# Optimization experiments

Hardware: AMD Instinct MI355X
Metric: run time of the kernel (lower is better)

## Reference

```python
import jax, jax.numpy as jnp
import numpy as np

N_NODES = 200_000
N_UND = 3_200_000        # undirected masked edges
E = 2 * N_UND            # directed edges


def _seg_mean(m, dst, n_nodes):
    # DGL fn.mean: mean over incoming edge messages; zero-in-degree nodes get 0.
    s = jax.ops.segment_sum(m, dst, num_segments=n_nodes)
    deg = jax.ops.segment_sum(jnp.ones((m.shape[0], 1), m.dtype), dst, num_segments=n_nodes)
    return s / jnp.maximum(deg, 1.0)


def setup_inputs() -> dict:
    key = jax.random.key(0)
    ks = jax.random.split(key, 18)
    w = lambda k, s: jax.random.normal(k, s, dtype=jnp.float32) * 0.1
    return {
        'node_feat': jax.random.normal(ks[0], (N_NODES, 7), dtype=jnp.float32),
        'edge_feat': jax.random.normal(ks[1], (E, 4), dtype=jnp.float32),
        'edge_mask': jax.random.normal(ks[2], (N_UND, 1), dtype=jnp.float32),
        'src': jax.random.randint(ks[3], (E,), 0, N_NODES),
        'dst': jax.random.randint(ks[4], (E,), 0, N_NODES),
        'W1a': w(ks[5], (11, 32)), 'b1a': jnp.zeros((32,), jnp.float32),
        'W1b': w(ks[6], (32, 32)), 'b1b': jnp.zeros((32,), jnp.float32),
        'W2a': w(ks[7], (32, 32)), 'b2a': jnp.zeros((32,), jnp.float32),
        'W2b': w(ks[8], (32, 32)), 'b2b': jnp.zeros((32,), jnp.float32),
        'Wm1': w(ks[9], (32, 16)), 'bm1': jnp.zeros((16,), jnp.float32),
        'Wm2': w(ks[10], (16, 2)), 'bm2': jnp.zeros((2,), jnp.float32),
    }


def reference(node_feat, edge_feat, edge_mask, src, dst,
              W1a, b1a, W1b, b1b, W2a, b2a, W2b, b2b, Wm1, bm1, Wm2, bm2):
    n_nodes = node_feat.shape[0]
    relu = jax.nn.relu
    # interleave mask to both edge directions: [m0, m0, m1, m1, ...]
    m_full = jax.nn.sigmoid(jnp.repeat(edge_mask, 2, axis=0))  # [E, 1]
    # layer 1: masked cat(edge_h, src_h) -> mean over dst -> MLP
    msg1 = m_full * jnp.concatenate([edge_feat, node_feat[src]], axis=1)  # [E, 11]
    h = _seg_mean(msg1, dst, n_nodes)                                      # [N, 11]
    h = relu(relu(h @ W1a + b1a) @ W1b + b1b)                              # [N, 32]
    # layer 2: masked src_h -> mean over dst -> MLP
    msg2 = m_full * h[src]                                                 # [E, 32]
    h = _seg_mean(msg2, dst, n_nodes)                                      # [N, 32]
    h = relu(relu(h @ W2a + b2a) @ W2b + b2b)                              # [N, 32]
    # global max pool + readout MLP + softmax (batch_size=1 path)
    g = jnp.max(h, axis=0)                                                 # [32]
    logits = relu(g @ Wm1 + bm1) @ Wm2 + bm2                               # [2]
    return jax.nn.softmax(logits)[None, :]                                 # [1, 2]
```

## Files before the change

kernel.cpp:

```cpp
#include <hip/hip_runtime.h>
#include <hip/hip_fp16.h>
#include <math.h>

#define SCHUNK 1024
#define PMAX   80
#define BSHIFT 9
#define MAXBKT 1024
#define BINB   1024
#define EPT    8

__device__ __forceinline__ float sigmoidf_(float x) {
    return 1.0f / (1.0f + __expf(-x));
}

union I2H { int i; __half2 h; };
__device__ __forceinline__ int pack_h2(float a, float b) {
    I2H u; u.h = __floats2half2_rn(a, b); return u.i;
}
__device__ __forceinline__ float2 unpack_h2(int w) {
    I2H u; u.i = w; return __half22float2(u.h);
}

typedef int v4i_nt __attribute__((ext_vector_type(4)));
typedef float v4f_nt __attribute__((ext_vector_type(4)));
__device__ __forceinline__ int4 ldnt16(const int4* p) {
    v4i_nt v = __builtin_nontemporal_load((const v4i_nt*)p);
    return make_int4(v[0], v[1], v[2], v[3]);
}
__device__ __forceinline__ float4 ldnt16f(const float* p) {
    v4f_nt v = __builtin_nontemporal_load((const v4f_nt*)p);
    return make_float4(v[0], v[1], v[2], v[3]);
}

__global__ void hist_rank(const int* __restrict__ dst, int* __restrict__ deg,
                          int* __restrict__ rank, int E) {
    int e = blockIdx.x * blockDim.x + threadIdx.x;
    if (e < E) rank[e] = atomicAdd(&deg[dst[e]], 1);
}

__global__ void scan_part(const int* __restrict__ deg, int* __restrict__ bsum, int N) {
    __shared__ int tot[256];
    int t = threadIdx.x;
    int base = blockIdx.x * SCHUNK + t * 4;
    int s = 0;
    if (base + 3 < N) {
        int4 v = *(const int4*)(deg + base);
        s = v.x + v.y + v.z + v.w;
    } else {
#pragma unroll
        for (int j = 0; j < 4; ++j) if (base + j < N) s += deg[base + j];
    }
    tot[t] = s;
    __syncthreads();
    for (int o = 128; o >= 1; o >>= 1) {
        if (t < o) tot[t] += tot[t + o];
        __syncthreads();
    }
    if (t == 0) bsum[blockIdx.x] = tot[0];
}

__global__ void scan_mid(int* __restrict__ bsum, int* __restrict__ off, int B, int N) {
    __shared__ int tmp[256];
    int t = threadIdx.x;
    int chunk = (B + 255) / 256;
    int lo = t * chunk, hi = min(lo + chunk, B);
    int s = 0;
    for (int i = lo; i < hi; ++i) s += bsum[i];
    tmp[t] = s;
    __syncthreads();
    for (int o = 1; o < 256; o <<= 1) {
        int v = (t >= o) ? tmp[t - o] : 0;
        __syncthreads();
        tmp[t] += v;
        __syncthreads();
    }
    int run = (t == 0) ? 0 : tmp[t - 1];
    for (int i = lo; i < hi; ++i) { int d = bsum[i]; bsum[i] = run; run += d; }
    if (t == 255) off[N] = tmp[255];
}

__global__ void scan_fin(const int* __restrict__ deg, const int* __restrict__ bsum,
                         int* __restrict__ off, int N) {
    __shared__ int tots[256];
    int t = threadIdx.x;
    int base = blockIdx.x * SCHUNK + t * 4;
    int v0 = 0, v1 = 0, v2 = 0, v3 = 0;
    if (base + 3 < N) {
        int4 v = *(const int4*)(deg + base);
        v0 = v.x; v1 = v.y; v2 = v.z; v3 = v.w;
    } else {
        if (base + 0 < N) v0 = deg[base + 0];
        if (base + 1 < N) v1 = deg[base + 1];
        if (base + 2 < N) v2 = deg[base + 2];
        if (base + 3 < N) v3 = deg[base + 3];
    }
    tots[t] = v0 + v1 + v2 + v3;
    __syncthreads();
    for (int o = 1; o < 256; o <<= 1) {
        int v = (t >= o) ? tots[t - o] : 0;
        __syncthreads();
        tots[t] += v;
        __syncthreads();
    }
    int run = bsum[blockIdx.x] + ((t == 0) ? 0 : tots[t - 1]);
    if (base + 0 < N) off[base + 0] = run; run += v0;
    if (base + 1 < N) off[base + 1] = run; run += v1;
    if (base + 2 < N) off[base + 2] = run; run += v2;
    if (base + 3 < N) off[base + 3] = run;
}

__global__ void pack_nodes(const float* __restrict__ nf, int4* __restrict__ nf16, int N) {
    int n = blockIdx.x * blockDim.x + threadIdx.x;
    if (n >= N) return;
    const float* p = nf + (size_t)n * 7;
    int4 w;
    w.x = pack_h2(p[0], p[1]);
    w.y = pack_h2(p[2], p[3]);
    w.z = pack_h2(p[4], p[5]);
    w.w = pack_h2(p[6], 0.0f);
    nf16[n] = w;
}

__global__ __launch_bounds__(BINB)
void binA(const int* __restrict__ dst, const int* __restrict__ src,
          const float* __restrict__ edge_mask, const float* __restrict__ edge_feat,
          const float* __restrict__ node_feat,
          int* __restrict__ bktCnt, int4* __restrict__ region, int4* __restrict__ nf16,
          int E, int N, int nbkt, int bcap) {
    __shared__ int cnt[MAXBKT];
    __shared__ int base[MAXBKT];
    int t = threadIdx.x;
    int gt = blockIdx.x * BINB + t;
    if (gt < N) {
        const float* p = node_feat + (size_t)gt * 7;
        int4 w;
        w.x = pack_h2(p[0], p[1]);
        w.y = pack_h2(p[2], p[3]);
        w.z = pack_h2(p[4], p[5]);
        w.w = pack_h2(p[6], 0.0f);
        nf16[gt] = w;
    }
    for (int i = t; i < nbkt; i += BINB) cnt[i] = 0;
    __syncthreads();
    int4 rec[EPT];
    int  bl[EPT];
    int e0 = blockIdx.x * (BINB * EPT) + t;
#pragma unroll
    for (int j = 0; j < EPT; ++j) {
        int e = e0 + j * BINB;
        bl[j] = -1;
        if (e < E) {
            int d = dst[e];
            int s = src[e];
            float m = sigmoidf_(edge_mask[e >> 1]);
            float4 ef = ldnt16f(edge_feat + (size_t)e * 4);
            int b = d >> BSHIFT;
            int dlo = d & ((1 << BSHIFT) - 1);
            int lr = atomicAdd(&cnt[b], 1);
            rec[j].x = (dlo << 18) | s;
            rec[j].y = pack_h2(m * ef.x, m * ef.y);
            rec[j].z = pack_h2(m * ef.z, m * ef.w);
            rec[j].w = __float_as_int(m);
            bl[j] = (b << 16) | lr;
        }
    }
    __syncthreads();
    for (int i = t; i < nbkt; i += BINB)
        base[i] = atomicAdd(&bktCnt[i], cnt[i]);
    __syncthreads();
#pragma unroll
    for (int j = 0; j < EPT; ++j) {
        if (bl[j] >= 0) {
            int b = bl[j] >> 16, lr = bl[j] & 0xffff;
            int pos = base[b] + lr;
            if (pos < bcap) region[(size_t)b * bcap + pos] = rec[j];
        }
    }
}

__global__ __launch_bounds__(1024)
void fillS(const int4* __restrict__ region, const int* __restrict__ bktCnt,
           int4* __restrict__ recP, int* __restrict__ deg, int N, int bcap) {
    __shared__ int cnt[1 << BSHIFT];
    int b = blockIdx.x;
    int t = threadIdx.x;
    if (t < (1 << BSHIFT)) cnt[t] = 0;
    __syncthreads();
    int count = min(bktCnt[b], bcap);
    const int4* reg = region + (size_t)b * bcap;
    int n0 = b << BSHIFT;
    for (int i = t; i < count; i += blockDim.x) {
        int4 w = ldnt16(reg + i);
        int dlo = ((unsigned)w.x) >> 18;
        int r = atomicAdd(&cnt[dlo], 1);
        if (r < PMAX) {
            w.x &= 0x3FFFF;
            recP[(size_t)(n0 + dlo) * PMAX + r] = w;
        }
    }
    __syncthreads();
    if (t < (1 << BSHIFT) && n0 + t < N) deg[n0 + t] = cnt[t];
}

__global__ void hist_fill_p(const int* __restrict__ dst, const int* __restrict__ src,
                            const float* __restrict__ edge_mask,
                            const float* __restrict__ edge_feat,
                            const float* __restrict__ node_feat,
                            int* __restrict__ deg, int4* __restrict__ recP,
                            int4* __restrict__ nf16, int E, int N) {
    int t = blockIdx.x * blockDim.x + threadIdx.x;
    if (t < N) {
        const float* p = node_feat + (size_t)t * 7;
        int4 w;
        w.x = pack_h2(p[0], p[1]);
        w.y = pack_h2(p[2], p[3]);
        w.z = pack_h2(p[4], p[5]);
        w.w = pack_h2(p[6], 0.0f);
        nf16[t] = w;
    }
    int e0 = blockIdx.x * (blockDim.x << 2) + threadIdx.x;
    int e1 = e0 + blockDim.x;
    int e2 = e1 + blockDim.x;
    int e3 = e2 + blockDim.x;
    bool v0 = e0 < E, v1 = e1 < E, v2 = e2 < E, v3 = e3 < E;
    int d0 = 0, d1 = 0, d2 = 0, d3 = 0;
    int s0 = 0, s1 = 0, s2 = 0, s3 = 0;
    float k0 = 0, k1 = 0, k2 = 0, k3 = 0;
    float4 f0 = {}, f1 = {}, f2 = {}, f3 = {};
    if (v0) { d0 = dst[e0]; s0 = src[e0]; k0 = edge_mask[e0 >> 1]; f0 = ldnt16f(edge_feat + (size_t)e0 * 4); }
    if (v1) { d1 = dst[e1]; s1 = src[e1]; k1 = edge_mask[e1 >> 1]; f1 = ldnt16f(edge_feat + (size_t)e1 * 4); }
    if (v2) { d2 = dst[e2]; s2 = src[e2]; k2 = edge_mask[e2 >> 1]; f2 = ldnt16f(edge_feat + (size_t)e2 * 4); }
    if (v3) { d3 = dst[e3]; s3 = src[e3]; k3 = edge_mask[e3 >> 1]; f3 = ldnt16f(edge_feat + (size_t)e3 * 4); }
    float m0 = sigmoidf_(k0), m1 = sigmoidf_(k1), m2 = sigmoidf_(k2), m3 = sigmoidf_(k3);
    int4 w0, w1, w2, w3;
    w0.x = s0; w0.y = pack_h2(m0 * f0.x, m0 * f0.y); w0.z = pack_h2(m0 * f0.z, m0 * f0.w); w0.w = __float_as_int(m0);
    w1.x = s1; w1.y = pack_h2(m1 * f1.x, m1 * f1.y); w1.z = pack_h2(m1 * f1.z, m1 * f1.w); w1.w = __float_as_int(m1);
    w2.x = s2; w2.y = pack_h2(m2 * f2.x, m2 * f2.y); w2.z = pack_h2(m2 * f2.z, m2 * f2.w); w2.w = __float_as_int(m2);
    w3.x = s3; w3.y = pack_h2(m3 * f3.x, m3 * f3.y); w3.z = pack_h2(m3 * f3.z, m3 * f3.w); w3.w = __float_as_int(m3);
    int r0 = 0, r1 = 0, r2 = 0, r3 = 0;
    if (v0) r0 = atomicAdd(&deg[d0], 1);
    if (v1) r1 = atomicAdd(&deg[d1], 1);
    if (v2) r2 = atomicAdd(&deg[d2], 1);
    if (v3) r3 = atomicAdd(&deg[d3], 1);
    if (v0 && r0 < PMAX) recP[(size_t)d0 * PMAX + r0] = w0;
    if (v1 && r1 < PMAX) recP[(size_t)d1 * PMAX + r1] = w1;
    if (v2 && r2 < PMAX) recP[(size_t)d2 * PMAX + r2] = w2;
    if (v3 && r3 < PMAX) recP[(size_t)d3 * PMAX + r3] = w3;
}

__global__ void agg1_p(const int4* __restrict__ recP, const int* __restrict__ degv,
                       const int4* __restrict__ nf16,
                       const float* __restrict__ W1a, const float* __restrict__ b1a,
                       const float* __restrict__ W1b, const float* __restrict__ b1b,
                       __half* __restrict__ h1h, int N) {
    __shared__ float sW1a[11 * 32], sb1a[32], sW1b[32 * 32], sb1b[32];
    for (int i = threadIdx.x; i < 11 * 32; i += blockDim.x) sW1a[i] = W1a[i];
    for (int i = threadIdx.x; i < 32 * 32; i += blockDim.x) sW1b[i] = W1b[i];
    if (threadIdx.x < 32) { sb1a[threadIdx.x] = b1a[threadIdx.x]; sb1b[threadIdx.x] = b1b[threadIdx.x]; }
    __syncthreads();
    int n = blockIdx.x * (blockDim.x >> 2) + (threadIdx.x >> 2);
    int sub = threadIdx.x & 3;
    int deg = 0;
    size_t start = 0;
    if (n < N) { deg = degv[n]; start = (size_t)n * PMAX; }
    int dd = min(deg, PMAX);
    float x[11];
#pragma unroll
    for (int j = 0; j < 11; ++j) x[j] = 0.0f;
    int i = sub;
    for (; i + 4 < dd; i += 8) {
        int4 r0 = ldnt16(recP + start + i);
        int4 r1 = ldnt16(recP + start + i + 4);
        int4 nw0 = nf16[r0.x];
        int4 nw1 = nf16[r1.x];
        {
            float m = __int_as_float(r0.w);
            float2 e01 = unpack_h2(r0.y), e23 = unpack_h2(r0.z);
            x[0] += e01.x; x[1] += e01.y; x[2] += e23.x; x[3] += e23.y;
            float2 n01 = unpack_h2(nw0.x), n23 = unpack_h2(nw0.y);
            float2 n45 = unpack_h2(nw0.z), n6 = unpack_h2(nw0.w);
            x[4] += m * n01.x; x[5]  += m * n01.y; x[6] += m * n23.x; x[7] += m * n23.y;
            x[8] += m * n45.x; x[9]  += m * n45.y; x[10] += m * n6.x;
        }
        {
// ... 82 lines not shown
        const int4* hp1 = (const int4*)(h1h + (size_t)r1.x * 32);
        int4 g00 = hp0[0], g01 = hp0[1], g02 = hp0[2], g03 = hp0[3];
        int4 g10 = hp1[0], g11 = hp1[1], g12 = hp1[2], g13 = hp1[3];
        {
            float m = __int_as_float(r0.w);
            float2 a, b, c, d;
            a = unpack_h2(g00.x); b = unpack_h2(g00.y); c = unpack_h2(g00.z); d = unpack_h2(g00.w);
            x[0] += m * a.x; x[1] += m * a.y; x[2] += m * b.x; x[3] += m * b.y;
            x[4] += m * c.x; x[5] += m * c.y; x[6] += m * d.x; x[7] += m * d.y;
            a = unpack_h2(g01.x); b = unpack_h2(g01.y); c = unpack_h2(g01.z); d = unpack_h2(g01.w);
            x[8] += m * a.x; x[9] += m * a.y; x[10] += m * b.x; x[11] += m * b.y;
            x[12] += m * c.x; x[13] += m * c.y; x[14] += m * d.x; x[15] += m * d.y;
            a = unpack_h2(g02.x); b = unpack_h2(g02.y); c = unpack_h2(g02.z); d = unpack_h2(g02.w);
            x[16] += m * a.x; x[17] += m * a.y; x[18] += m * b.x; x[19] += m * b.y;
            x[20] += m * c.x; x[21] += m * c.y; x[22] += m * d.x; x[23] += m * d.y;
            a = unpack_h2(g03.x); b = unpack_h2(g03.y); c = unpack_h2(g03.z); d = unpack_h2(g03.w);
            x[24] += m * a.x; x[25] += m * a.y; x[26] += m * b.x; x[27] += m * b.y;
            x[28] += m * c.x; x[29] += m * c.y; x[30] += m * d.x; x[31] += m * d.y;
        }
        {
            float m = __int_as_float(r1.w);
            float2 a, b, c, d;
            a = unpack_h2(g10.x); b = unpack_h2(g10.y); c = unpack_h2(g10.z); d = unpack_h2(g10.w);
            x[0] += m * a.x; x[1] += m * a.y; x[2] += m * b.x; x[3] += m * b.y;
            x[4] += m * c.x; x[5] += m * c.y; x[6] += m * d.x; x[7] += m * d.y;
            a = unpack_h2(g11.x); b = unpack_h2(g11.y); c = unpack_h2(g11.z); d = unpack_h2(g11.w);
            x[8] += m * a.x; x[9] += m * a.y; x[10] += m * b.x; x[11] += m * b.y;
            x[12] += m * c.x; x[13] += m * c.y; x[14] += m * d.x; x[15] += m * d.y;
            a = unpack_h2(g12.x); b = unpack_h2(g12.y); c = unpack_h2(g12.z); d = unpack_h2(g12.w);
            x[16] += m * a.x; x[17] += m * a.y; x[18] += m * b.x; x[19] += m * b.y;
            x[20] += m * c.x; x[21] += m * c.y; x[22] += m * d.x; x[23] += m * d.y;
            a = unpack_h2(g13.x); b = unpack_h2(g13.y); c = unpack_h2(g13.z); d = unpack_h2(g13.w);
            x[24] += m * a.x; x[25] += m * a.y; x[26] += m * b.x; x[27] += m * b.y;
            x[28] += m * c.x; x[29] += m * c.y; x[30] += m * d.x; x[31] += m * d.y;
        }
    }
    for (; i < dd; i += 4) {
        int4 r = ldnt16(recP + start + i);
        float m = __int_as_float(r.w);
        const int4* hp = (const int4*)(h1h + (size_t)r.x * 32);
#pragma unroll
        for (int q = 0; q < 4; ++q) {
            int4 v = hp[q];
            float2 a = unpack_h2(v.x), b = unpack_h2(v.y);
            float2 c = unpack_h2(v.z), d = unpack_h2(v.w);
            x[8 * q + 0] += m * a.x; x[8 * q + 1] += m * a.y;
            x[8 * q + 2] += m * b.x; x[8 * q + 3] += m * b.y;
            x[8 * q + 4] += m * c.x; x[8 * q + 5] += m * c.y;
            x[8 * q + 6] += m * d.x; x[8 * q + 7] += m * d.y;
        }
    }
#pragma unroll
    for (int j = 0; j < 32; ++j) {
        x[j] += __shfl_xor(x[j], 1);
        x[j] += __shfl_xor(x[j], 2);
    }
    float inv = 1.0f / fmaxf((float)deg, 1.0f);
#pragma unroll
    for (int j = 0; j < 32; ++j) x[j] *= inv;
    float hdn[32];
#pragma unroll
    for (int k = 0; k < 32; ++k) {
        float acc = sb2a[k];
#pragma unroll
        for (int j = 0; j < 32; ++j) acc += x[j] * sW2a[j * 32 + k];
        hdn[k] = fmaxf(acc, 0.0f);
    }
    int lane = threadIdx.x & 63;
#pragma unroll
    for (int k2 = 0; k2 < 32; ++k2) {
        float acc = sb2b[k2];
#pragma unroll
        for (int k = 0; k < 32; ++k) acc += hdn[k] * sW2b[k * 32 + k2];
        float v = valid ? fmaxf(acc, 0.0f) : 0.0f;
#pragma unroll
        for (int o = 32; o >= 1; o >>= 1)
            v = fmaxf(v, __shfl_xor(v, o));
        if (lane == 0) atomicMax(&smax[k2], __float_as_int(v));
    }
    __syncthreads();
    if (threadIdx.x < 32) atomicMax((int*)&gmax[threadIdx.x], smax[threadIdx.x]);
}

__global__ void fill_rec16(const int* __restrict__ dst, const int* __restrict__ rank,
                           const int* __restrict__ off,
                           const float* __restrict__ edge_mask,
                           const int* __restrict__ src,
                           const float* __restrict__ edge_feat,
                           int4* __restrict__ rec, int E) {
    int e = blockIdx.x * blockDim.x + threadIdx.x;
    if (e >= E) return;
    int p = off[dst[e]] + rank[e];
    float m = sigmoidf_(edge_mask[e >> 1]);
    float4 ef = ldnt16f(edge_feat + (size_t)e * 4);
    int4 w;
    w.x = src[e];
    w.y = pack_h2(m * ef.x, m * ef.y);
    w.z = pack_h2(m * ef.z, m * ef.w);
    w.w = __float_as_int(m);
    rec[p] = w;
}

__global__ void agg1_16(const int4* __restrict__ rec, const int* __restrict__ off,
                        const int4* __restrict__ nf16,
                        const float* __restrict__ W1a, const float* __restrict__ b1a,
                        const float* __restrict__ W1b, const float* __restrict__ b1b,
                        __half* __restrict__ h1h, int N) {
    __shared__ float sW1a[11 * 32], sb1a[32], sW1b[32 * 32], sb1b[32];
    for (int i = threadIdx.x; i < 11 * 32; i += blockDim.x) sW1a[i] = W1a[i];
    for (int i = threadIdx.x; i < 32 * 32; i += blockDim.x) sW1b[i] = W1b[i];
    if (threadIdx.x < 32) { sb1a[threadIdx.x] = b1a[threadIdx.x]; sb1b[threadIdx.x] = b1b[threadIdx.x]; }
    __syncthreads();
    int n = blockIdx.x * (blockDim.x >> 2) + (threadIdx.x >> 2);
    int sub = threadIdx.x & 3;
    int start = 0, deg = 0;
    if (n < N) { start = off[n]; deg = off[n + 1] - start; }
    float x[11];
#pragma unroll
    for (int j = 0; j < 11; ++j) x[j] = 0.0f;
    for (int i = sub; i < deg; i += 4) {
        int4 r = ldnt16(rec + start + i);
        float m = __int_as_float(r.w);
        float2 e01 = unpack_h2(r.y), e23 = unpack_h2(r.z);
        x[0] += e01.x; x[1] += e01.y; x[2] += e23.x; x[3] += e23.y;
        int4 nw = nf16[r.x];
        float2 n01 = unpack_h2(nw.x), n23 = unpack_h2(nw.y);
        float2 n45 = unpack_h2(nw.z), n6 = unpack_h2(nw.w);
        x[4] += m * n01.x; x[5]  += m * n01.y; x[6] += m * n23.x; x[7] += m * n23.y;
        x[8] += m * n45.x; x[9]  += m * n45.y; x[10] += m * n6.x;
    }
#pragma unroll
    for (int j = 0; j < 11; ++j) {
        x[j] += __shfl_xor(x[j], 1);
        x[j] += __shfl_xor(x[j], 2);
    }
    if (n >= N) return;
    float inv = 1.0f / fmaxf((float)deg, 1.0f);
#pragma unroll
    for (int j = 0; j < 11; ++j) x[j] *= inv;
    float hdn[32];
#pragma unroll
    for (int k = 0; k < 32; ++k) {
        float acc = sb1a[k];
#pragma unroll
        for (int j = 0; j < 11; ++j) acc += x[j] * sW1a[j * 32 + k];
        hdn[k] = fmaxf(acc, 0.0f);
    }
    float o[32];
#pragma unroll
    for (int k2 = 0; k2 < 32; ++k2) {
        float acc = sb1b[k2];
#pragma unroll
        for (int k = 0; k < 32; ++k) acc += hdn[k] * sW1b[k * 32 + k2];
        o[k2] = fmaxf(acc, 0.0f);
    }
    int4 w;
    w.x = pack_h2(o[8 * sub + 0], o[8 * sub + 1]);
    w.y = pack_h2(o[8 * sub + 2], o[8 * sub + 3]);
    w.z = pack_h2(o[8 * sub + 4], o[8 * sub + 5]);
    w.w = pack_h2(o[8 * sub + 6], o[8 * sub + 7]);
    ((int4*)(h1h + (size_t)n * 32))[sub] = w;
}

__global__ void agg2_16(const int4* __restrict__ rec, const int* __restrict__ off,
                        const __half* __restrict__ h1h,
                        const float* __restrict__ W2a, const float* __restrict__ b2a,
                        const float* __restrict__ W2b, const float* __restrict__ b2b,
                        float* __restrict__ gmax, int N) {
    __shared__ float sW2a[32 * 32], sb2a[32], sW2b[32 * 32], sb2b[32];
    __shared__ int smax[32];
    for (int i = threadIdx.x; i < 32 * 32; i += blockDim.x) { sW2a[i] = W2a[i]; sW2b[i] = W2b[i]; }
    if (threadIdx.x < 32) {
        sb2a[threadIdx.x] = b2a[threadIdx.x];
        sb2b[threadIdx.x] = b2b[threadIdx.x];
        smax[threadIdx.x] = 0;
    }
    __syncthreads();
    int n = blockIdx.x * (blockDim.x >> 2) + (threadIdx.x >> 2);
    int sub = threadIdx.x & 3;
    bool valid = (n < N);
    int start = 0, deg = 0;
    if (valid) { start = off[n]; deg = off[n + 1] - start; }
    float x[32];
#pragma unroll
    for (int j = 0; j < 32; ++j) x[j] = 0.0f;
    for (int i = sub; i < deg; i += 4) {
        int4 r = ldnt16(rec + start + i);
        float m = __int_as_float(r.w);
        const int4* hp = (const int4*)(h1h + (size_t)r.x * 32);
#pragma unroll
        for (int q = 0; q < 4; ++q) {
            int4 v = hp[q];
            float2 a = unpack_h2(v.x), b = unpack_h2(v.y);
            float2 c = unpack_h2(v.z), d = unpack_h2(v.w);
            x[8 * q + 0] += m * a.x; x[8 * q + 1] += m * a.y;
            x[8 * q + 2] += m * b.x; x[8 * q + 3] += m * b.y;
            x[8 * q + 4] += m * c.x; x[8 * q + 5] += m * c.y;
            x[8 * q + 6] += m * d.x; x[8 * q + 7] += m * d.y;
        }
    }
#pragma unroll
    for (int j = 0; j < 32; ++j) {
        x[j] += __shfl_xor(x[j], 1);
        x[j] += __shfl_xor(x[j], 2);
    }
    float inv = 1.0f / fmaxf((float)deg, 1.0f);
#pragma unroll
    for (int j = 0; j < 32; ++j) x[j] *= inv;
    float hdn[32];
#pragma unroll
    for (int k = 0; k < 32; ++k) {
        float acc = sb2a[k];
#pragma unroll
        for (int j = 0; j < 32; ++j) acc += x[j] * sW2a[j * 32 + k];
        hdn[k] = fmaxf(acc, 0.0f);
    }
    int lane = threadIdx.x & 63;
#pragma unroll
    for (int k2 = 0; k2 < 32; ++k2) {
        float acc = sb2b[k2];
#pragma unroll
        for (int k = 0; k < 32; ++k) acc += hdn[k] * sW2b[k * 32 + k2];
        float v = valid ? fmaxf(acc, 0.0f) : 0.0f;
#pragma unroll
        for (int o = 32; o >= 1; o >>= 1)
            v = fmaxf(v, __shfl_xor(v, o));
        if (lane == 0) atomicMax(&smax[k2], __float_as_int(v));
    }
    __syncthreads();
    if (threadIdx.x < 32) atomicMax((int*)&gmax[threadIdx.x], smax[threadIdx.x]);
}

__global__ void fill_rec(const int* __restrict__ dst, const int* __restrict__ rank,
                         const int* __restrict__ off,
                         const float* __restrict__ edge_mask,
                         const int* __restrict__ src,
                         int2* __restrict__ rec, int E) {
    int e = blockIdx.x * blockDim.x + threadIdx.x;
    if (e >= E) return;
    int p = off[dst[e]] + rank[e];
    float m = sigmoidf_(edge_mask[e >> 1]);
    int mq = (int)(m * 16384.0f + 0.5f);
    mq = min(mq, 16383);
    unsigned packed = ((unsigned)src[e] << 14) | (unsigned)mq;
    rec[p] = make_int2(e, (int)packed);
}

__global__ void agg1_rec(const int2* __restrict__ rec, const int* __restrict__ off,
                         const float* __restrict__ edge_feat,
                         const float* __restrict__ node_feat,
                         const float* __restrict__ W1a, const float* __restrict__ b1a,
                         const float* __restrict__ W1b, const float* __restrict__ b1b,
                         float* __restrict__ h1, int N) {
    __shared__ float sW1a[11 * 32], sb1a[32], sW1b[32 * 32], sb1b[32];
    for (int i = threadIdx.x; i < 11 * 32; i += blockDim.x) sW1a[i] = W1a[i];
    for (int i = threadIdx.x; i < 32 * 32; i += blockDim.x) sW1b[i] = W1b[i];
    if (threadIdx.x < 32) { sb1a[threadIdx.x] = b1a[threadIdx.x]; sb1b[threadIdx.x] = b1b[threadIdx.x]; }
    __syncthreads();
    int n = blockIdx.x * blockDim.x + threadIdx.x;
    if (n >= N) return;
    int start = off[n];
    int deg = off[n + 1] - start;
    float x[11];
#pragma unroll
    for (int j = 0; j < 11; ++j) x[j] = 0.0f;
    for (int i = 0; i < deg; ++i) {
        int2 r = rec[start + i];
        int e = r.x;
        unsigned packed = (unsigned)r.y;
        int s = (int)(packed >> 14);
        float m = (float)(packed & 16383u) * (1.0f / 16384.0f);
        float4 ef = *(const float4*)(edge_feat + (size_t)e * 4);
        x[0] += m * ef.x; x[1] += m * ef.y; x[2] += m * ef.z; x[3] += m * ef.w;
        const float* nf = node_feat + (size_t)s * 7;
#pragma unroll
        for (int j = 0; j < 7; ++j) x[4 + j] += m * nf[j];
    }
    float inv = 1.0f / fmaxf((float)deg, 1.0f);
#pragma unroll
    for (int j = 0; j < 11; ++j) x[j] *= inv;
    float hdn[32];
#pragma unroll
    for (int k = 0; k < 32; ++k) {
        float acc = sb1a[k];
#pragma unroll
        for (int j = 0; j < 11; ++j) acc += x[j] * sW1a[j * 32 + k];
        hdn[k] = fmaxf(acc, 0.0f);
    }
    float o[32];
#pragma unroll
    for (int k2 = 0; k2 < 32; ++k2) {
        float acc = sb1b[k2];
#pragma unroll
        for (int k = 0; k < 32; ++k) acc += hdn[k] * sW1b[k * 32 + k2];
        o[k2] = fmaxf(acc, 0.0f);
    }
    float4* outp = (float4*)(h1 + (size_t)n * 32);
#pragma unroll
    for (int q = 0; q < 8; ++q)
        outp[q] = make_float4(o[4 * q], o[4 * q + 1], o[4 * q + 2], o[4 * q + 3]);
}

__global__ void agg2_rec(const int2* __restrict__ rec, const int* __restrict__ off,
                         const float* __restrict__ h1,
                         const float* __restrict__ W2a, const float* __restrict__ b2a,
                         const float* __restrict__ W2b, const float* __restrict__ b2b,
                         float* __restrict__ gmax, int N) {
    __shared__ float sW2a[32 * 32], sb2a[32], sW2b[32 * 32], sb2b[32];
    __shared__ int smax[32];
    for (int i = threadIdx.x; i < 32 * 32; i += blockDim.x) { sW2a[i] = W2a[i]; sW2b[i] = W2b[i]; }
    if (threadIdx.x < 32) {
        sb2a[threadIdx.x] = b2a[threadIdx.x];
        sb2b[threadIdx.x] = b2b[threadIdx.x];
        smax[threadIdx.x] = 0;
    }
// ... 17 lines not shown
            float4 v = hp[q];
            x[4 * q + 0] += m * v.x;
            x[4 * q + 1] += m * v.y;
            x[4 * q + 2] += m * v.z;
            x[4 * q + 3] += m * v.w;
        }
    }
    float inv = 1.0f / fmaxf((float)deg, 1.0f);
#pragma unroll
    for (int j = 0; j < 32; ++j) x[j] *= inv;
    float hdn[32];
#pragma unroll
    for (int k = 0; k < 32; ++k) {
        float acc = sb2a[k];
#pragma unroll
        for (int j = 0; j < 32; ++j) acc += x[j] * sW2a[j * 32 + k];
        hdn[k] = fmaxf(acc, 0.0f);
    }
    int lane = threadIdx.x & 63;
#pragma unroll
    for (int k2 = 0; k2 < 32; ++k2) {
        float acc = sb2b[k2];
#pragma unroll
        for (int k = 0; k < 32; ++k) acc += hdn[k] * sW2b[k * 32 + k2];
        float v = valid ? fmaxf(acc, 0.0f) : 0.0f;
#pragma unroll
        for (int o = 32; o >= 1; o >>= 1)
            v = fmaxf(v, __shfl_xor(v, o));
        if (lane == 0) atomicMax(&smax[k2], __float_as_int(v));
    }
    __syncthreads();
    if (threadIdx.x < 32) atomicMax((int*)&gmax[threadIdx.x], smax[threadIdx.x]);
}

__global__ void readout(const float* __restrict__ gmax,
                        const float* __restrict__ Wm1, const float* __restrict__ bm1,
                        const float* __restrict__ Wm2, const float* __restrict__ bm2,
                        float* __restrict__ out) {
    __shared__ float p[16];
    int t = threadIdx.x;
    if (t < 16) {
        float acc = bm1[t];
        for (int j = 0; j < 32; ++j) acc += gmax[j] * Wm1[j * 16 + t];
        p[t] = fmaxf(acc, 0.0f);
    }
    __syncthreads();
    if (t == 0) {
        float l0 = bm2[0], l1 = bm2[1];
        for (int k = 0; k < 16; ++k) { l0 += p[k] * Wm2[k * 2]; l1 += p[k] * Wm2[k * 2 + 1]; }
        float mx = fmaxf(l0, l1);
        float e0 = __expf(l0 - mx), e1 = __expf(l1 - mx);
        float s = e0 + e1;
        out[0] = e0 / s;
        out[1] = e1 / s;
    }
}

static inline size_t align16(size_t x) { return (x + 15) & ~(size_t)15; }

extern "C" void kernel_launch(void* const* d_in, const int* in_sizes, int n_in,
                              void* d_out, int out_size, void* d_ws, size_t ws_size,
                              hipStream_t stream) {
    const float* node_feat = (const float*)d_in[0];
    const float* edge_feat = (const float*)d_in[1];
    const float* edge_mask = (const float*)d_in[2];
    const int*   src       = (const int*)d_in[3];
    const int*   dst       = (const int*)d_in[4];
    const float* W1a = (const float*)d_in[5];
    const float* b1a = (const float*)d_in[6];
    const float* W1b = (const float*)d_in[7];
    const float* b1b = (const float*)d_in[8];
    const float* W2a = (const float*)d_in[9];
    const float* b2a = (const float*)d_in[10];
    const float* W2b = (const float*)d_in[11];
    const float* b2b = (const float*)d_in[12];
    const float* Wm1 = (const float*)d_in[13];
    const float* bm1 = (const float*)d_in[14];
    const float* Wm2 = (const float*)d_in[15];
    const float* bm2 = (const float*)d_in[16];

    const int N = in_sizes[0] / 7;
    const int E = in_sizes[3];
    const int B = (N + SCHUNK - 1) / SCHUNK;

    {
        const int nbkt = (N + (1 << BSHIFT) - 1) >> BSHIFT;
        if (nbkt <= MAXBKT && N <= (1 << 18)) {
            int avg = (E + nbkt - 1) / nbkt;
            int bcap = avg + avg / 8 + 256;
            char* basep = (char*)d_ws;
            size_t off0 = 0;
            int*   bktCnt = (int*)(basep + off0);  off0 += (size_t)(nbkt + 32) * sizeof(int);
            float* gmax   = (float*)(bktCnt + nbkt);
            off0 = align16(off0);
            int*   degS   = (int*)(basep + off0);  off0 += (size_t)N * sizeof(int);
            off0 = align16(off0);
            int4*  nf16   = (int4*)(basep + off0); off0 += (size_t)N * sizeof(int4);
            int4*  recP   = (int4*)(basep + off0); off0 += (size_t)N * PMAX * sizeof(int4);
            int4*  region = (int4*)(basep + off0);
            __half* h1h   = (__half*)region;
            size_t regionBytes = (size_t)nbkt * bcap * sizeof(int4);
            size_t h1Bytes = (size_t)N * 32 * sizeof(__half);
            off0 += (regionBytes > h1Bytes ? regionBytes : h1Bytes);
            const size_t needS = off0;
            if (ws_size >= needS) {
                hipMemsetAsync(d_ws, 0, (size_t)(nbkt + 32) * sizeof(int), stream);
                const int binBlocks = (max(E, N) + BINB * EPT - 1) / (BINB * EPT);
                binA<<<binBlocks, BINB, 0, stream>>>(dst, src, edge_mask, edge_feat, node_feat,
                                                     bktCnt, region, nf16, E, N, nbkt, bcap);
                fillS<<<nbkt, 1024, 0, stream>>>(region, bktCnt, recP, degS, N, bcap);
                const int nodeBlocks = (N + 63) / 64;
                agg1_p<<<nodeBlocks, 256, 0, stream>>>(recP, degS, nf16,
                                                       W1a, b1a, W1b, b1b, h1h, N);
                agg2_p<<<nodeBlocks, 256, 0, stream>>>(recP, degS, h1h,
                                                       W2a, b2a, W2b, b2b, gmax, N);
                readout<<<1, 64, 0, stream>>>(gmax, Wm1, bm1, Wm2, bm2, (float*)d_out);
                return;
            }
        }
    }

    {
        int*    deg_i = (int*)d_ws;
        float*  gmax  = (float*)(deg_i + N);
        __half* h1h   = (__half*)(gmax + 32);
        int4*   nf16  = (int4*)(h1h + (size_t)N * 32);
        int4*   recP  = nf16 + N;
        const size_t needP = (size_t)(deg_i + N + 32 - (int*)d_ws) * sizeof(int)
                           + (size_t)N * 32 * sizeof(__half)
                           + (size_t)N * sizeof(int4)
                           + (size_t)N * PMAX * sizeof(int4);
        if (ws_size >= needP) {
            hipMemsetAsync(d_ws, 0, (size_t)(N + 32) * sizeof(int), stream);
            int threadsNeeded = max((E + 3) / 4, N);
            const int gridEF = (threadsNeeded + 255) / 256;
            hist_fill_p<<<gridEF, 256, 0, stream>>>(dst, src, edge_mask, edge_feat,
                                                    node_feat, deg_i, recP, nf16, E, N);
            const int nodeBlocks = (N + 63) / 64;
            agg1_p<<<nodeBlocks, 256, 0, stream>>>(recP, deg_i, nf16,
                                                   W1a, b1a, W1b, b1b, h1h, N);
            agg2_p<<<nodeBlocks, 256, 0, stream>>>(recP, deg_i, h1h,
                                                   W2a, b2a, W2b, b2b, gmax, N);
            readout<<<1, 64, 0, stream>>>(gmax, Wm1, bm1, Wm2, bm2, (float*)d_out);
            return;
        }
    }

    int*   deg_i = (int*)d_ws;
    float* gmax  = (float*)(deg_i + N);
    int*   off   = (int*)(gmax + 32);
    int*   bsum  = off + (N + 1);
    int*   slot  = bsum + (B + 1);

    const size_t slot16 = (size_t)E > (size_t)16 * N ? (size_t)E : (size_t)16 * N;
    int*    rank   = slot;
    __half* h1h    = (__half*)slot;
    int4*   rec16  = (int4*)(slot + slot16);
    int4*   nf16   = rec16 + E;
    const size_t need16 = ((size_t)2 * N + 34 + B + slot16 + (size_t)E * 4 + (size_t)N * 4) * sizeof(int);

    const size_t slot8 = (size_t)E > (size_t)32 * N ? (size_t)E : (size_t)32 * N;
    float* h1f  = (float*)slot;
    int2*  rec8 = (int2*)(slot + slot8);

    hipMemsetAsync(d_ws, 0, (size_t)(N + 32) * sizeof(int), stream);

    hist_rank<<<(E + 255) / 256, 256, 0, stream>>>(dst, deg_i, rank, E);
    scan_part<<<B, 256, 0, stream>>>(deg_i, bsum, N);
    scan_mid<<<1, 256, 0, stream>>>(bsum, off, B, N);
    scan_fin<<<B, 256, 0, stream>>>(deg_i, bsum, off, N);

    if (ws_size >= need16) {
        const int nodeBlocks = (N + 63) / 64;
        pack_nodes<<<(N + 255) / 256, 256, 0, stream>>>(node_feat, nf16, N);
        fill_rec16<<<(E + 255) / 256, 256, 0, stream>>>(dst, rank, off, edge_mask, src,
                                                        edge_feat, rec16, E);
        agg1_16<<<nodeBlocks, 256, 0, stream>>>(rec16, off, nf16,
                                                W1a, b1a, W1b, b1b, h1h, N);
        agg2_16<<<nodeBlocks, 256, 0, stream>>>(rec16, off, h1h,
                                                W2a, b2a, W2b, b2b, gmax, N);
    } else {
        fill_rec<<<(E + 255) / 256, 256, 0, stream>>>(dst, rank, off, edge_mask, src, rec8, E);
        agg1_rec<<<(N + 255) / 256, 256, 0, stream>>>(rec8, off, edge_feat, node_feat,
                                                      W1a, b1a, W1b, b1b, h1f, N);
        agg2_rec<<<(N + 255) / 256, 256, 0, stream>>>(rec8, off, h1f,
                                                      W2a, b2a, W2b, b2b, gmax, N);
    }
    readout<<<1, 64, 0, stream>>>(gmax, Wm1, bm1, Wm2, bm2, (float*)d_out);
}
```

Before: 668.3 us.

## Aggregate directly from dst buckets with LDS atomics, dropping the per-node fill pass

Adds agg1R/agg2R, which have one 1024-thread block per 512-node destination bucket. Each block reads the binned edge records straight from the bucket region and accumulates messages and degree into shared-memory rows with float atomics, then runs the per-node MLPs. This removes the fillS scatter into a padded per-node record array (N*PMAX int4) and its extra global traffic, and also lifts the PMAX cap on in-degree. In exchange it adds heavy LDS atomic contention (up to 33 atomics per edge in layer 2), uses only 512 of 1024 threads for the MLP phase, and makes float summation order nondeterministic. It also deletes the unused rec16 fallback path.

```diff
diff --git a/kernel.cpp b/kernel.cpp
--- a/kernel.cpp
+++ b/kernel.cpp
@@ -5,6 +5,7 @@
 #define SCHUNK 1024
 #define PMAX   80
 #define BSHIFT 9
+#define RB     (1 << BSHIFT)
 #define MAXBKT 1024
 #define BINB   1024
 #define EPT    8
@@ -107,18 +108,6 @@
     if (base + 1 < N) off[base + 1] = run; run += v1;
     if (base + 2 < N) off[base + 2] = run; run += v2;
     if (base + 3 < N) off[base + 3] = run;
-}
-
-__global__ void pack_nodes(const float* __restrict__ nf, int4* __restrict__ nf16, int N) {
-    int n = blockIdx.x * blockDim.x + threadIdx.x;
-    if (n >= N) return;
-    const float* p = nf + (size_t)n * 7;
-    int4 w;
-    w.x = pack_h2(p[0], p[1]);
-    w.y = pack_h2(p[2], p[3]);
-    w.z = pack_h2(p[4], p[5]);
-    w.w = pack_h2(p[6], 0.0f);
-    nf16[n] = w;
 }
 
 __global__ __launch_bounds__(BINB)
@@ -155,7 +144,7 @@
             float m = sigmoidf_(edge_mask[e >> 1]);
             float4 ef = ldnt16f(edge_feat + (size_t)e * 4);
             int b = d >> BSHIFT;
-            int dlo = d & ((1 << BSHIFT) - 1);
+            int dlo = d & (RB - 1);
             int lr = atomicAdd(&cnt[b], 1);
             rec[j].x = (dlo << 18) | s;
             rec[j].y = pack_h2(m * ef.x, m * ef.y);
@@ -179,12 +168,168 @@
 }
 
 __global__ __launch_bounds__(1024)
+void agg1R(const int4* __restrict__ region, const int* __restrict__ bktCnt,
+           const int4* __restrict__ nf16,
+           const float* __restrict__ W1a, const float* __restrict__ b1a,
+           const float* __restrict__ W1b, const float* __restrict__ b1b,
+           __half* __restrict__ h1h, int N, int bcap) {
+    __shared__ float xs[RB * 13];
+    __shared__ float sW1a[11 * 32], sb1a[32], sW1b[32 * 32], sb1b[32];
+    int t = threadIdx.x;
+    for (int i = t; i < 11 * 32; i += 1024) sW1a[i] = W1a[i];
+    for (int i = t; i < 32 * 32; i += 1024) sW1b[i] = W1b[i];
+    if (t < 32) { sb1a[t] = b1a[t]; sb1b[t] = b1b[t]; }
+    for (int i = t; i < RB * 13; i += 1024) xs[i] = 0.0f;
+    __syncthreads();
+    int b = blockIdx.x;
+    int count = min(bktCnt[b], bcap);
+    const int4* reg = region + (size_t)b * bcap;
+    for (int i = t; i < count; i += 1024) {
+        int4 w = ldnt16(reg + i);
+        int dlo = ((unsigned)w.x) >> 18;
+        int s = w.x & 0x3FFFF;
+        float m = __int_as_float(w.w);
+        float2 e01 = unpack_h2(w.y), e23 = unpack_h2(w.z);
+        int4 nw = nf16[s];
+        float2 n01 = unpack_h2(nw.x), n23 = unpack_h2(nw.y);
+        float2 n45 = unpack_h2(nw.z), n6 = unpack_h2(nw.w);
+        float* xp = xs + dlo * 13;
+        atomicAdd(xp + 0, e01.x);  atomicAdd(xp + 1, e01.y);
+        atomicAdd(xp + 2, e23.x);  atomicAdd(xp + 3, e23.y);
+        atomicAdd(xp + 4, m * n01.x);  atomicAdd(xp + 5, m * n01.y);
+        atomicAdd(xp + 6, m * n23.x);  atomicAdd(xp + 7, m * n23.y);
+        atomicAdd(xp + 8, m * n45.x);  atomicAdd(xp + 9, m * n45.y);
+        atomicAdd(xp + 10, m * n6.x);
+        atomicAdd(xp + 11, 1.0f);
+    }
+    __syncthreads();
+    int n0 = b << BSHIFT;
+    if (t < RB && n0 + t < N) {
+        float inv = 1.0f / fmaxf(xs[t * 13 + 11], 1.0f);
+        float hdn[32];
+#pragma unroll
+        for (int k = 0; k < 32; ++k) hdn[k] = sb1a[k];
+#pragma unroll
+        for (int j = 0; j < 11; ++j) {
+            float xv = xs[t * 13 + j] * inv;
+#pragma unroll
+            for (int k = 0; k < 32; ++k) hdn[k] += xv * sW1a[j * 32 + k];
+        }
+#pragma unroll
+        for (int k = 0; k < 32; ++k) hdn[k] = fmaxf(hdn[k], 0.0f);
+        int4* outp = (int4*)(h1h + (size_t)(n0 + t) * 32);
+#pragma unroll
+        for (int q = 0; q < 4; ++q) {
+            float o0 = sb1b[q * 8 + 0], o1 = sb1b[q * 8 + 1], o2 = sb1b[q * 8 + 2], o3 = sb1b[q * 8 + 3];
+            float o4 = sb1b[q * 8 + 4], o5 = sb1b[q * 8 + 5], o6 = sb1b[q * 8 + 6], o7 = sb1b[q * 8 + 7];
+#pragma unroll
+            for (int k = 0; k < 32; ++k) {
+                float hk = hdn[k];
+                const float* wr = sW1b + k * 32 + q * 8;
+                o0 += hk * wr[0]; o1 += hk * wr[1]; o2 += hk * wr[2]; o3 += hk * wr[3];
+                o4 += hk * wr[4]; o5 += hk * wr[5]; o6 += hk * wr[6]; o7 += hk * wr[7];
+            }
+            int4 w;
+            w.x = pack_h2(fmaxf(o0, 0.0f), fmaxf(o1, 0.0f));
+            w.y = pack_h2(fmaxf(o2, 0.0f), fmaxf(o3, 0.0f));
+            w.z = pack_h2(fmaxf(o4, 0.0f), fmaxf(o5, 0.0f));
+            w.w = pack_h2(fmaxf(o6, 0.0f), fmaxf(o7, 0.0f));
+            outp[q] = w;
+        }
+    }
+}
+
+__global__ __launch_bounds__(1024)
+void agg2R(const int4* __restrict__ region, const int* __restrict__ bktCnt,
+           const __half* __restrict__ h1h,
+           const float* __restrict__ W2a, const float* __restrict__ b2a,
+           const float* __restrict__ W2b, const float* __restrict__ b2b,
+           float* __restrict__ gmax, int N, int bcap) {
+    __shared__ float xs[RB * 33];
+    __shared__ float sW2a[32 * 32], sb2a[32], sW2b[32 * 32], sb2b[32];
+    __shared__ int smax[32];
+    int t = threadIdx.x;
+    for (int i = t; i < 32 * 32; i += 1024) { sW2a[i] = W2a[i]; sW2b[i] = W2b[i]; }
+    if (t < 32) { sb2a[t] = b2a[t]; sb2b[t] = b2b[t]; smax[t] = 0; }
+    for (int i = t; i < RB * 33; i += 1024) xs[i] = 0.0f;
+    __syncthreads();
+    int b = blockIdx.x;
+    int count = min(bktCnt[b], bcap);
+    const int4* reg = region + (size_t)b * bcap;
+    for (int i = t; i < count; i += 1024) {
+        int4 w = ldnt16(reg + i);
+        int dlo = ((unsigned)w.x) >> 18;
+        int s = w.x & 0x3FFFF;
+        float m = __int_as_float(w.w);
+        const int4* hp = (const int4*)(h1h + (size_t)s * 32);
+        int4 g0 = hp[0], g1 = hp[1], g2 = hp[2], g3 = hp[3];
+        float* xp = xs + dlo * 33;
+        float2 a, c;
+        a = unpack_h2(g0.x); c = unpack_h2(g0.y);
+        atomicAdd(xp + 0, m * a.x); atomicAdd(xp + 1, m * a.y);
+        atomicAdd(xp + 2, m * c.x); atomicAdd(xp + 3, m * c.y);
+        a = unpack_h2(g0.z); c = unpack_h2(g0.w);
+        atomicAdd(xp + 4, m * a.x); atomicAdd(xp + 5, m * a.y);
+        atomicAdd(xp + 6, m * c.x); atomicAdd(xp + 7, m * c.y);
+        a = unpack_h2(g1.x); c = unpack_h2(g1.y);
+        atomicAdd(xp + 8, m * a.x); atomicAdd(xp + 9, m * a.y);
+        atomicAdd(xp + 10, m * c.x); atomicAdd(xp + 11, m * c.y);
+        a = unpack_h2(g1.z); c = unpack_h2(g1.w);
+        atomicAdd(xp + 12, m * a.x); atomicAdd(xp + 13, m * a.y);
+        atomicAdd(xp + 14, m * c.x); atomicAdd(xp + 15, m * c.y);
+        a = unpack_h2(g2.x); c = unpack_h2(g2.y);
+        atomicAdd(xp + 16, m * a.x); atomicAdd(xp + 17, m * a.y);
+        atomicAdd(xp + 18, m * c.x); atomicAdd(xp + 19, m * c.y);
+        a = unpack_h2(g2.z); c = unpack_h2(g2.w);
+        atomicAdd(xp + 20, m * a.x); atomicAdd(xp + 21, m * a.y);
+        atomicAdd(xp + 22, m * c.x); atomicAdd(xp + 23, m * c.y);
+        a = unpack_h2(g3.x); c = unpack_h2(g3.y);
+        atomicAdd(xp + 24, m * a.x); atomicAdd(xp + 25, m * a.y);
+        atomicAdd(xp + 26, m * c.x); atomicAdd(xp + 27, m * c.y);
+        a = unpack_h2(g3.z); c = unpack_h2(g3.w);
+        atomicAdd(xp + 28, m * a.x); atomicAdd(xp + 29, m * a.y);
+        atomicAdd(xp + 30, m * c.x); atomicAdd(xp + 31, m * c.y);
+        atomicAdd(xp + 32, 1.0f);
+    }
+    __syncthreads();
+    int n0 = b << BSHIFT;
+    if (t < RB) {
+        bool valid = (n0 + t < N);
+        float inv = 1.0f / fmaxf(xs[t * 33 + 32], 1.0f);
+        float hdn[32];
+#pragma unroll
+        for (int k = 0; k < 32; ++k) hdn[k] = sb2a[k];
+#pragma unroll
+        for (int j = 0; j < 32; ++j) {
+            float xv = xs[t * 33 + j] * inv;
+#pragma unroll
+            for (int k = 0; k < 32; ++k) hdn[k] += xv * sW2a[j * 32 + k];
+        }
+#pragma unroll
+        for (int k = 0; k < 32; ++k) hdn[k] = fmaxf(hdn[k], 0.0f);
+#pragma unroll
+        for (int k2 = 0; k2 < 32; ++k2) {
+            float acc = sb2b[k2];
+#pragma unroll
+            for (int k = 0; k < 32; ++k) acc += hdn[k] * sW2b[k * 32 + k2];
+            float v = valid ? fmaxf(acc, 0.0f) : 0.0f;
+#pragma unroll
+            for (int o = 32; o >= 1; o >>= 1)
+                v = fmaxf(v, __shfl_xor(v, o));
+            if ((t & 63) == 0) atomicMax(&smax[k2], __float_as_int(v));
+        }
+    }
+    __syncthreads();
+    if (t < 32) atomicMax((int*)&gmax[t], smax[t]);
+}
+
+__global__ __launch_bounds__(1024)
 void fillS(const int4* __restrict__ region, const int* __restrict__ bktCnt,
            int4* __restrict__ recP, int* __restrict__ deg, int N, int bcap) {
-    __shared__ int cnt[1 << BSHIFT];
+    __shared__ int cnt[RB];
     int b = blockIdx.x;
     int t = threadIdx.x;
-    if (t < (1 << BSHIFT)) cnt[t] = 0;
+    if (t < RB) cnt[t] = 0;
     __syncthreads();
     int count = min(bktCnt[b], bcap);
     const int4* reg = region + (size_t)b * bcap;
@@ -199,7 +344,7 @@
         }
     }
     __syncthreads();
-    if (t < (1 << BSHIFT) && n0 + t < N) deg[n0 + t] = cnt[t];
+    if (t < RB && n0 + t < N) deg[n0 + t] = cnt[t];
 }
 
 __global__ void hist_fill_p(const int* __restrict__ dst, const int* __restrict__ src,
@@ -448,155 +593,6 @@
     if (threadIdx.x < 32) atomicMax((int*)&gmax[threadIdx.x], smax[threadIdx.x]);
 }
 
-__global__ void fill_rec16(const int* __restrict__ dst, const int* __restrict__ rank,
-                           const int* __restrict__ off,
-                           const float* __restrict__ edge_mask,
-                           const int* __restrict__ src,
-                           const float* __restrict__ edge_feat,
-                           int4* __restrict__ rec, int E) {
-    int e = blockIdx.x * blockDim.x + threadIdx.x;
-    if (e >= E) return;
-    int p = off[dst[e]] + rank[e];
-    float m = sigmoidf_(edge_mask[e >> 1]);
-    float4 ef = ldnt16f(edge_feat + (size_t)e * 4);
-    int4 w;
-    w.x = src[e];
-    w.y = pack_h2(m * ef.x, m * ef.y);
-    w.z = pack_h2(m * ef.z, m * ef.w);
-    w.w = __float_as_int(m);
-    rec[p] = w;
-}
-
-__global__ void agg1_16(const int4* __restrict__ rec, const int* __restrict__ off,
-                        const int4* __restrict__ nf16,
-                        const float* __restrict__ W1a, const float* __restrict__ b1a,
-                        const float* __restrict__ W1b, const float* __restrict__ b1b,
-                        __half* __restrict__ h1h, int N) {
-    __shared__ float sW1a[11 * 32], sb1a[32], sW1b[32 * 32], sb1b[32];
-    for (int i = threadIdx.x; i < 11 * 32; i += blockDim.x) sW1a[i] = W1a[i];
-    for (int i = threadIdx.x; i < 32 * 32; i += blockDim.x) sW1b[i] = W1b[i];
-    if (threadIdx.x < 32) { sb1a[threadIdx.x] = b1a[threadIdx.x]; sb1b[threadIdx.x] = b1b[threadIdx.x]; }
-    __syncthreads();
-    int n = blockIdx.x * (blockDim.x >> 2) + (threadIdx.x >> 2);
-    int sub = threadIdx.x & 3;
-    int start = 0, deg = 0;
-    if (n < N) { start = off[n]; deg = off[n + 1] - start; }
-    float x[11];
-#pragma unroll
-    for (int j = 0; j < 11; ++j) x[j] = 0.0f;
-    for (int i = sub; i < deg; i += 4) {
-        int4 r = ldnt16(rec + start + i);
-        float m = __int_as_float(r.w);
-        float2 e01 = unpack_h2(r.y), e23 = unpack_h2(r.z);
-        x[0] += e01.x; x[1] += e01.y; x[2] += e23.x; x[3] += e23.y;
-        int4 nw = nf16[r.x];
-        float2 n01 = unpack_h2(nw.x), n23 = unpack_h2(nw.y);
-        float2 n45 = unpack_h2(nw.z), n6 = unpack_h2(nw.w);
-        x[4] += m * n01.x; x[5]  += m * n01.y; x[6] += m * n23.x; x[7] += m * n23.y;
-        x[8] += m * n45.x; x[9]  += m * n45.y; x[10] += m * n6.x;
-    }
-#pragma unroll
-    for (int j = 0; j < 11; ++j) {
-        x[j] += __shfl_xor(x[j], 1);
-        x[j] += __shfl_xor(x[j], 2);
-    }
-    if (n >= N) return;
-    float inv = 1.0f / fmaxf((float)deg, 1.0f);
-#pragma unroll
-    for (int j = 0; j < 11; ++j) x[j] *= inv;
-    float hdn[32];
-#pragma unroll
-    for (int k = 0; k < 32; ++k) {
-        float acc = sb1a[k];
-#pragma unroll
-        for (int j = 0; j < 11; ++j) acc += x[j] * sW1a[j * 32 + k];
-        hdn[k] = fmaxf(acc, 0.0f);
-    }
-    float o[32];
-#pragma unroll
-    for (int k2 = 0; k2 < 32; ++k2) {
-        float acc = sb1b[k2];
-#pragma unroll
-        for (int k = 0; k < 32; ++k) acc += hdn[k] * sW1b[k * 32 + k2];
-        o[k2] = fmaxf(acc, 0.0f);
-    }
-    int4 w;
-    w.x = pack_h2(o[8 * sub + 0], o[8 * sub + 1]);
-    w.y = pack_h2(o[8 * sub + 2], o[8 * sub + 3]);
-    w.z = pack_h2(o[8 * sub + 4], o[8 * sub + 5]);
-    w.w = pack_h2(o[8 * sub + 6], o[8 * sub + 7]);
-    ((int4*)(h1h + (size_t)n * 32))[sub] = w;
-}
-
-__global__ void agg2_16(const int4* __restrict__ rec, const int* __restrict__ off,
-                        const __half* __restrict__ h1h,
-                        const float* __restrict__ W2a, const float* __restrict__ b2a,
-                        const float* __restrict__ W2b, const float* __restrict__ b2b,
-                        float* __restrict__ gmax, int N) {
-    __shared__ float sW2a[32 * 32], sb2a[32], sW2b[32 * 32], sb2b[32];
-    __shared__ int smax[32];
-    for (int i = threadIdx.x; i < 32 * 32; i += blockDim.x) { sW2a[i] = W2a[i]; sW2b[i] = W2b[i]; }
-    if (threadIdx.x < 32) {
-        sb2a[threadIdx.x] = b2a[threadIdx.x];
-        sb2b[threadIdx.x] = b2b[threadIdx.x];
-        smax[threadIdx.x] = 0;
-    }
-    __syncthreads();
-    int n = blockIdx.x * (blockDim.x >> 2) + (threadIdx.x >> 2);
-    int sub = threadIdx.x & 3;
-    bool valid = (n < N);
-    int start = 0, deg = 0;
-    if (valid) { start = off[n]; deg = off[n + 1] - start; }
-    float x[32];
-#pragma unroll
-    for (int j = 0; j < 32; ++j) x[j] = 0.0f;
-    for (int i = sub; i < deg; i += 4) {
-        int4 r = ldnt16(rec + start + i);
-        float m = __int_as_float(r.w);
-        const int4* hp = (const int4*)(h1h + (size_t)r.x * 32);
-#pragma unroll
-        for (int q = 0; q < 4; ++q) {
-            int4 v = hp[q];
-            float2 a = unpack_h2(v.x), b = unpack_h2(v.y);
-            float2 c = unpack_h2(v.z), d = unpack_h2(v.w);
-            x[8 * q + 0] += m * a.x; x[8 * q + 1] += m * a.y;
-            x[8 * q + 2] += m * b.x; x[8 * q + 3] += m * b.y;
-            x[8 * q + 4] += m * c.x; x[8 * q + 5] += m * c.y;
-            x[8 * q + 6] += m * d.x; x[8 * q + 7] += m * d.y;
-        }
-    }
-#pragma unroll
-    for (int j = 0; j < 32; ++j) {
-        x[j] += __shfl_xor(x[j], 1);
-        x[j] += __shfl_xor(x[j], 2);
-    }
-    float inv = 1.0f / fmaxf((float)deg, 1.0f);
-#pragma unroll
-    for (int j = 0; j < 32; ++j) x[j] *= inv;
-    float hdn[32];
-#pragma unroll
-    for (int k = 0; k < 32; ++k) {
-        float acc = sb2a[k];
-#pragma unroll
-        for (int j = 0; j < 32; ++j) acc += x[j] * sW2a[j * 32 + k];
-        hdn[k] = fmaxf(acc, 0.0f);
-    }
-    int lane = threadIdx.x & 63;
-#pragma unroll
-    for (int k2 = 0; k2 < 32; ++k2) {
-        float acc = sb2b[k2];
-#pragma unroll
-        for (int k = 0; k < 32; ++k) acc += hdn[k] * sW2b[k * 32 + k2];
-        float v = valid ? fmaxf(acc, 0.0f) : 0.0f;
-#pragma unroll
-        for (int o = 32; o >= 1; o >>= 1)
-            v = fmaxf(v, __shfl_xor(v, o));
-        if (lane == 0) atomicMax(&smax[k2], __float_as_int(v));
-    }
-    __syncthreads();
-    if (threadIdx.x < 32) atomicMax((int*)&gmax[threadIdx.x], smax[threadIdx.x]);
-}
-
 __global__ void fill_rec(const int* __restrict__ dst, const int* __restrict__ rank,
                          const int* __restrict__ off,
                          const float* __restrict__ edge_mask,
@@ -780,41 +776,64 @@
     const int N = in_sizes[0] / 7;
     const int E = in_sizes[3];
     const int B = (N + SCHUNK - 1) / SCHUNK;
-
-    {
-        const int nbkt = (N + (1 << BSHIFT) - 1) >> BSHIFT;
-        if (nbkt <= MAXBKT && N <= (1 << 18)) {
-            int avg = (E + nbkt - 1) / nbkt;
-            int bcap = avg + avg / 8 + 256;
-            char* basep = (char*)d_ws;
-            size_t off0 = 0;
-            int*   bktCnt = (int*)(basep + off0);  off0 += (size_t)(nbkt + 32) * sizeof(int);
-            float* gmax   = (float*)(bktCnt + nbkt);
-            off0 = align16(off0);
-            int*   degS   = (int*)(basep + off0);  off0 += (size_t)N * sizeof(int);
-            off0 = align16(off0);
-            int4*  nf16   = (int4*)(basep + off0); off0 += (size_t)N * sizeof(int4);
-            int4*  recP   = (int4*)(basep + off0); off0 += (size_t)N * PMAX * sizeof(int4);
-            int4*  region = (int4*)(basep + off0);
-            __half* h1h   = (__half*)region;
-            size_t regionBytes = (size_t)nbkt * bcap * sizeof(int4);
-            size_t h1Bytes = (size_t)N * 32 * sizeof(__half);
-            off0 += (regionBytes > h1Bytes ? regionBytes : h1Bytes);
-            const size_t needS = off0;
-            if (ws_size >= needS) {
-                hipMemsetAsync(d_ws, 0, (size_t)(nbkt + 32) * sizeof(int), stream);
-                const int binBlocks = (max(E, N) + BINB * EPT - 1) / (BINB * EPT);
-                binA<<<binBlocks, BINB, 0, stream>>>(dst, src, edge_mask, edge_feat, node_feat,
-                                                     bktCnt, region, nf16, E, N, nbkt, bcap);
-                fillS<<<nbkt, 1024, 0, stream>>>(region, bktCnt, recP, degS, N, bcap);
-                const int nodeBlocks = (N + 63) / 64;
-                agg1_p<<<nodeBlocks, 256, 0, stream>>>(recP, degS, nf16,
-                                                       W1a, b1a, W1b, b1b, h1h, N);
-                agg2_p<<<nodeBlocks, 256, 0, stream>>>(recP, degS, h1h,
-                                                       W2a, b2a, W2b, b2b, gmax, N);
-                readout<<<1, 64, 0, stream>>>(gmax, Wm1, bm1, Wm2, bm2, (float*)d_out);
-                return;
-            }
+    const int nbkt = (N + RB - 1) >> BSHIFT;
+    const int avg = (E + nbkt - 1) / nbkt;
+    const int bcap = avg + avg / 8 + 256;
+
+    if (nbkt <= MAXBKT && N <= (1 << 18)) {
+        char* basep = (char*)d_ws;
+        size_t off0 = 0;
+        int*   bktCnt = (int*)(basep + off0);  off0 += (size_t)(nbkt + 32) * sizeof(int);
+        float* gmax   = (float*)(bktCnt + nbkt);
+        off0 = align16(off0);
+        int4*  nf16   = (int4*)(basep + off0); off0 += (size_t)N * sizeof(int4);
+        __half* h1h   = (__half*)(basep + off0); off0 += (size_t)N * 32 * sizeof(__half);
+        off0 = align16(off0);
+        int4*  region = (int4*)(basep + off0); off0 += (size_t)nbkt * bcap * sizeof(int4);
+        const size_t needR = off0;
+        if (ws_size >= needR) {
+            hipMemsetAsync(d_ws, 0, (size_t)(nbkt + 32) * sizeof(int), stream);
+            const int binBlocks = (max(E, N) + BINB * EPT - 1) / (BINB * EPT);
+            binA<<<binBlocks, BINB, 0, stream>>>(dst, src, edge_mask, edge_feat, node_feat,
+                                                 bktCnt, region, nf16, E, N, nbkt, bcap);
+            agg1R<<<nbkt, 1024, 0, stream>>>(region, bktCnt, nf16,
+                                             W1a, b1a, W1b, b1b, h1h, N, bcap);
+            agg2R<<<nbkt, 1024, 0, stream>>>(region, bktCnt, h1h,
+                                             W2a, b2a, W2b, b2b, gmax, N, bcap);
+            readout<<<1, 64, 0, stream>>>(gmax, Wm1, bm1, Wm2, bm2, (float*)d_out);
+            return;
+        }
+    }
+
+    if (nbkt <= MAXBKT && N <= (1 << 18)) {
+        char* basep = (char*)d_ws;
+        size_t off0 = 0;
+        int*   bktCnt = (int*)(basep + off0);  off0 += (size_t)(nbkt + 32) * sizeof(int);
+        float* gmax   = (float*)(bktCnt + nbkt);
+        off0 = align16(off0);
+        int*   degS   = (int*)(basep + off0);  off0 += (size_t)N * sizeof(int);
+        off0 = align16(off0);
+        int4*  nf16   = (int4*)(basep + off0); off0 += (size_t)N * sizeof(int4);
+        int4*  recP   = (int4*)(basep + off0); off0 += (size_t)N * PMAX * sizeof(int4);
+        int4*  region = (int4*)(basep + off0);
+        __half* h1h   = (__half*)region;
+        size_t regionBytes = (size_t)nbkt * bcap * sizeof(int4);
+        size_t h1Bytes = (size_t)N * 32 * sizeof(__half);
+        off0 += (regionBytes > h1Bytes ? regionBytes : h1Bytes);
+        const size_t needS = off0;
+        if (ws_size >= needS) {
+            hipMemsetAsync(d_ws, 0, (size_t)(nbkt + 32) * sizeof(int), stream);
+            const int binBlocks = (max(E, N) + BINB * EPT - 1) / (BINB * EPT);
+            binA<<<binBlocks, BINB, 0, stream>>>(dst, src, edge_mask, edge_feat, node_feat,
+                                                 bktCnt, region, nf16, E, N, nbkt, bcap);
+            fillS<<<nbkt, 1024, 0, stream>>>(region, bktCnt, recP, degS, N, bcap);
+            const int nodeBlocks = (N + 63) / 64;
+            agg1_p<<<nodeBlocks, 256, 0, stream>>>(recP, degS, nf16,
+                                                   W1a, b1a, W1b, b1b, h1h, N);
+            agg2_p<<<nodeBlocks, 256, 0, stream>>>(recP, degS, h1h,
+                                                   W2a, b2a, W2b, b2b, gmax, N);
+            readout<<<1, 64, 0, stream>>>(gmax, Wm1, bm1, Wm2, bm2, (float*)d_out);
+            return;
         }
     }
 
@@ -849,40 +868,20 @@
     int*   off   = (int*)(gmax + 32);
     int*   bsum  = off + (N + 1);
     int*   slot  = bsum + (B + 1);
-
-    const size_t slot16 = (size_t)E > (size_t)16 * N ? (size_t)E : (size_t)16 * N;
-    int*    rank   = slot;
-    __half* h1h    = (__half*)slot;
-    int4*   rec16  = (int4*)(slot + slot16);
-    int4*   nf16   = rec16 + E;
-    const size_t need16 = ((size_t)2 * N + 34 + B + slot16 + (size_t)E * 4 + (size_t)N * 4) * sizeof(int);
-
     const size_t slot8 = (size_t)E > (size_t)32 * N ? (size_t)E : (size_t)32 * N;
+    int*   rank = slot;
     float* h1f  = (float*)slot;
     int2*  rec8 = (int2*)(slot + slot8);
 
     hipMemsetAsync(d_ws, 0, (size_t)(N + 32) * sizeof(int), stream);
-
     hist_rank<<<(E + 255) / 256, 256, 0, stream>>>(dst, deg_i, rank, E);
     scan_part<<<B, 256, 0, stream>>>(deg_i, bsum, N);
     scan_mid<<<1, 256, 0, stream>>>(bsum, off, B, N);
     scan_fin<<<B, 256, 0, stream>>>(deg_i, bsum, off, N);
-
-    if (ws_size >= need16) {
-        const int nodeBlocks = (N + 63) / 64;
-        pack_nodes<<<(N + 255) / 256, 256, 0, stream>>>(node_feat, nf16, N);
-        fill_rec16<<<(E + 255) / 256, 256, 0, stream>>>(dst, rank, off, edge_mask, src,
-                                                        edge_feat, rec16, E);
-        agg1_16<<<nodeBlocks, 256, 0, stream>>>(rec16, off, nf16,
-                                                W1a, b1a, W1b, b1b, h1h, N);
-        agg2_16<<<nodeBlocks, 256, 0, stream>>>(rec16, off, h1h,
-                                                W2a, b2a, W2b, b2b, gmax, N);
-    } else {
-        fill_rec<<<(E + 255) / 256, 256, 0, stream>>>(dst, rank, off, edge_mask, src, rec8, E);
-        agg1_rec<<<(N + 255) / 256, 256, 0, stream>>>(rec8, off, edge_feat, node_feat,
-                                                      W1a, b1a, W1b, b1b, h1f, N);
-        agg2_rec<<<(N + 255) / 256, 256, 0, stream>>>(rec8, off, h1f,
-                                                      W2a, b2a, W2b, b2b, gmax, N);
-    }
+    fill_rec<<<(E + 255) / 256, 256, 0, stream>>>(dst, rank, off, edge_mask, src, rec8, E);
+    agg1_rec<<<(N + 255) / 256, 256, 0, stream>>>(rec8, off, edge_feat, node_feat,
+                                                  W1a, b1a, W1b, b1b, h1f, N);
+    agg2_rec<<<(N + 255) / 256, 256, 0, stream>>>(rec8, off, h1f,
+                                                  W2a, b2a, W2b, b2b, gmax, N);
     readout<<<1, 64, 0, stream>>>(gmax, Wm1, bm1, Wm2, bm2, (float*)d_out);
 }
```

After: 2.241 ms. +235.3%, slower.
